# Kernel tuning notes

Measured on AMD Instinct MI355X. Metric: run time of the kernel, lower is better.

## Reference

```python
import jax, jax.numpy as jnp
import numpy as np

B, T, D, H = 2, 2048, 1024, 16
HD = D // H  # head dim = 64

def build_rope(t, half, base=10000.0):
    inv = 1.0 / (base ** (jnp.arange(0, half, dtype=jnp.float32) / half))
    ang = jnp.arange(t, dtype=jnp.float32)[:, None] * inv[None, :]  # (T, half)
    return jnp.stack([jnp.cos(ang), jnp.sin(ang)], axis=-1)  # (T, half, 2)

def setup_inputs() -> dict:
    key = jax.random.key(0)
    k1, k2, k3 = jax.random.split(key, 3)
    x = jax.random.normal(k1, (B, T, D), dtype=jnp.float32)
    W_attn = jax.random.normal(k2, (D, 3 * D), dtype=jnp.float32) * (1.0 / np.sqrt(D))
    W_proj = jax.random.normal(k3, (D, D), dtype=jnp.float32) * (1.0 / np.sqrt(D))
    rope = build_rope(T, HD // 2)
    mask = jnp.tril(jnp.ones((T, T), dtype=bool))[None, None]  # (1,1,T,T) causal
    return {"x": x, "rope": rope, "W_attn": W_attn, "W_proj": W_proj, "mask": mask}

def apply_rope(xq, rope):
    # xq: (B, T, H, HD); rope: (T, HD//2, 2)
    xs = xq.astype(jnp.float32).reshape(*xq.shape[:-1], -1, 2)        # (B,T,H,HD/2,2)
    rc = rope[:xq.shape[1]].reshape(1, xq.shape[1], 1, xs.shape[3], 2)  # (1,T,1,HD/2,2)
    out = jnp.stack([
        xs[..., 0] * rc[..., 0] - xs[..., 1] * rc[..., 1],
        xs[..., 1] * rc[..., 0] + xs[..., 0] * rc[..., 1],
    ], axis=-1)
    return out.reshape(xq.shape).astype(xq.dtype)

def reference(x, rope, W_attn, W_proj, mask):
    b, t, d = x.shape
    qkv = x @ W_attn                                   # (B,T,3D)
    q, k, v = jnp.split(qkv, 3, axis=2)
    q = apply_rope(q.reshape(b, t, H, HD), rope)
    k = apply_rope(k.reshape(b, t, H, HD), rope)
    v = v.reshape(b, t, H, HD)
    # (B,H,T,HD)
    q = q.transpose(0, 2, 1, 3)
    k = k.transpose(0, 2, 1, 3)
    v = v.transpose(0, 2, 1, 3)
    scale = 1.0 / np.sqrt(HD)
    scores = jnp.einsum('bhqd,bhkd->bhqk', q, k) * scale
    scores = jnp.where(mask, scores, jnp.finfo(scores.dtype).min)
    attn = jax.nn.softmax(scores, axis=-1)
    out = jnp.einsum('bhqk,bhkd->bhqd', attn, v)       # (B,H,T,HD)
    out = out.transpose(0, 2, 1, 3).reshape(b, t, d)
    return out @ W_proj
```

## Files before the change

kernel.cpp:

```cpp
#include <hip/hip_runtime.h>


typedef __bf16 bf16x8 __attribute__((ext_vector_type(8)));
typedef float f32x4 __attribute__((ext_vector_type(4)));

__device__ __forceinline__ float bf2f(unsigned short u) {
  unsigned int i = ((unsigned int)u) << 16;
  return __builtin_bit_cast(float, i);
}
__device__ __forceinline__ unsigned short f2bf(float f) {
  unsigned int i = __builtin_bit_cast(unsigned int, f);
  i += 0x7FFFu + ((i >> 16) & 1u);
  return (unsigned short)(i >> 16);
}
__device__ __forceinline__ unsigned int pack2(float a, float b) {
  return (unsigned int)f2bf(a) | ((unsigned int)f2bf(b) << 16);
}
__device__ __forceinline__ unsigned int cvtpk(float a, float b) {
  unsigned int r;
  asm("v_cvt_pk_bf16_f32 %0, %1, %2" : "=v"(r) : "v"(a), "v"(b));
  return r;
}

__device__ __forceinline__ void gload_lds16(const unsigned short* g, unsigned short* l) {
  __builtin_amdgcn_global_load_lds(
      (const __attribute__((address_space(1))) void*)g,
      (__attribute__((address_space(3))) void*)l, 16, 0, 0);
}

__global__ __launch_bounds__(256) void prep_kernel(
    const float* __restrict__ x, unsigned short* __restrict__ xb,
    const float* __restrict__ Wa, unsigned short* __restrict__ WaT,
    const float* __restrict__ Wp, unsigned short* __restrict__ WpT)
{
  __shared__ unsigned short tileT[64][72];
  const int bid = blockIdx.x, tid = threadIdx.x;

  if (bid < 2048) {
    int i = bid * 256 + tid;
    const float4 a0 = *reinterpret_cast<const float4*>(&x[(size_t)i * 8]);
    const float4 a1 = *reinterpret_cast<const float4*>(&x[(size_t)i * 8 + 4]);
    uint4 pk;
    pk.x = pack2(a0.x, a0.y);
    pk.y = pack2(a0.z, a0.w);
    pk.z = pack2(a1.x, a1.y);
    pk.w = pack2(a1.z, a1.w);
    *reinterpret_cast<uint4*>(&xb[(size_t)i * 8]) = pk;
    return;
  }
  const float* W;
  unsigned short* WT;
  int R, C, c0, r0;
  if (bid < 2816) {
    int tb = bid - 2048;
    W = Wa; WT = WaT; R = 1024; C = 3072;
    c0 = (tb % 48) * 64; r0 = (tb / 48) * 64;
  } else {
    int tb = bid - 2816;
    W = Wp; WT = WpT; R = 1024; C = 1024;
    c0 = (tb % 16) * 64; r0 = (tb / 16) * 64;
  }
  const int rr = tid >> 4, cc = (tid & 15) * 4;
#pragma unroll
  for (int it = 0; it < 4; ++it) {
    int gr = r0 + rr + it * 16;
    float4 v = *reinterpret_cast<const float4*>(&W[(size_t)gr * C + c0 + cc]);
    tileT[cc + 0][rr + it * 16] = f2bf(v.x);
    tileT[cc + 1][rr + it * 16] = f2bf(v.y);
    tileT[cc + 2][rr + it * 16] = f2bf(v.z);
    tileT[cc + 3][rr + it * 16] = f2bf(v.w);
  }
  __syncthreads();
  const int wc = tid >> 2, wk = (tid & 3) * 16;
  uint4 o0 = *reinterpret_cast<const uint4*>(&tileT[wc][wk]);
  uint4 o1 = *reinterpret_cast<const uint4*>(&tileT[wc][wk + 8]);
  unsigned short* dst = &WT[(size_t)(c0 + wc) * R + r0 + wk];
  *reinterpret_cast<uint4*>(dst) = o0;
  *reinterpret_cast<uint4*>(dst + 8) = o1;
}

__global__ __launch_bounds__(256) void gemm_qkv_kernel(
    const unsigned short* __restrict__ A, const unsigned short* __restrict__ BT,
    const float* __restrict__ rope,
    unsigned short* __restrict__ Qb, unsigned short* __restrict__ Kb,
    unsigned short* __restrict__ VT, int M, int N, int K)
{
  __shared__ alignas(16) unsigned short smem[16896];
  unsigned short* As = smem;
  unsigned short* Bs = smem + 4096;

  const int tid = threadIdx.x;
  const int nbx = gridDim.x;
  const int nwg = nbx * gridDim.y;
  const int orig = blockIdx.y * nbx + blockIdx.x;
  const int wg = (orig & 7) * (nwg >> 3) + (orig >> 3);
  const int m0 = (wg / nbx) * 128, n0 = (wg % nbx) * 128;

  const int w = tid >> 6, lane = tid & 63;
  const int wr = (w >> 1) * 64, wc = (w & 1) * 64;
  const int g = lane >> 4, r = lane & 15;

  f32x4 acc[4][4];
#pragma unroll
  for (int i = 0; i < 4; ++i)
#pragma unroll
    for (int j = 0; j < 4; ++j)
      acc[i][j] = f32x4{0.f, 0.f, 0.f, 0.f};

  const int srow = w * 32 + (lane >> 2);
  const int sk = (lane & 3) << 3;
  const size_t a_base = (size_t)(m0 + srow) * K + sk;
  const size_t b_base = (size_t)(n0 + srow) * K + sk;
  unsigned short* lA = &As[w * 1024 + lane * 8];
  unsigned short* lB = &Bs[w * 1024 + lane * 8];
  const size_t rstep = (size_t)16 * K;

  for (int k0 = 0; k0 < K; k0 += 32) {
    __syncthreads();
    gload_lds16(&A[a_base + k0], lA);
    gload_lds16(&A[a_base + k0 + rstep], lA + 512);
    gload_lds16(&BT[b_base + k0], lB);
    gload_lds16(&BT[b_base + k0 + rstep], lB + 512);
    __syncthreads();

    bf16x8 af[4], bff[4];
#pragma unroll
    for (int i = 0; i < 4; ++i)
      af[i] = __builtin_bit_cast(bf16x8,
          *reinterpret_cast<const uint4*>(&As[(wr + i * 16 + r) * 32 + g * 8]));
#pragma unroll
    for (int j = 0; j < 4; ++j)
      bff[j] = __builtin_bit_cast(bf16x8,
          *reinterpret_cast<const uint4*>(&Bs[(wc + j * 16 + r) * 32 + g * 8]));
#pragma unroll
    for (int i = 0; i < 4; ++i)
#pragma unroll
      for (int j = 0; j < 4; ++j)
        acc[i][j] = __builtin_amdgcn_mfma_f32_16x16x32_bf16(af[i], bff[j], acc[i][j], 0, 0, 0);
  }

  __syncthreads();
  unsigned short* ct = smem;
#pragma unroll
  for (int i = 0; i < 4; ++i)
#pragma unroll
    for (int j = 0; j < 4; ++j) {
      int row0 = wr + i * 16 + g * 4;
      int col  = wc + j * 16 + r;
      unsigned int w01 = cvtpk(acc[i][j][0], acc[i][j][1]);
      unsigned int w23 = cvtpk(acc[i][j][2], acc[i][j][3]);
      ct[(row0 + 0) * 132 + col] = (unsigned short)(w01 & 0xffffu);
      ct[(row0 + 1) * 132 + col] = (unsigned short)(w01 >> 16);
      ct[(row0 + 2) * 132 + col] = (unsigned short)(w23 & 0xffffu);
      ct[(row0 + 3) * 132 + col] = (unsigned short)(w23 >> 16);
    }
  __syncthreads();

  const int sec = n0 >> 10;
  if (sec < 2) {
    unsigned short* dstp = (sec == 0) ? Qb : Kb;
    const int prow = tid >> 4, pcol = (tid & 15) * 8;
    const int h = ((n0 & 1023) + pcol) >> 6;
    const int hd = pcol & 63;
#pragma unroll
    for (int p = 0; p < 8; ++p) {
      int row = p * 16 + prow;
      int rowM = m0 + row;
      int bb = rowM >> 11, tt = rowM & 2047;
      uint4 v = *reinterpret_cast<const uint4*>(&ct[row * 132 + pcol]);
      float x0 = bf2f((unsigned short)(v.x & 0xffffu)), x1 = bf2f((unsigned short)(v.x >> 16));
      float x2 = bf2f((unsigned short)(v.y & 0xffffu)), x3 = bf2f((unsigned short)(v.y >> 16));
      float x4 = bf2f((unsigned short)(v.z & 0xffffu)), x5 = bf2f((unsigned short)(v.z >> 16));
      float x6 = bf2f((unsigned short)(v.w & 0xffffu)), x7 = bf2f((unsigned short)(v.w >> 16));
      float4 rc0 = *reinterpret_cast<const float4*>(&rope[(size_t)tt * 64 + hd]);
      float4 rc1 = *reinterpret_cast<const float4*>(&rope[(size_t)tt * 64 + hd + 4]);
      float y0 = x0 * rc0.x - x1 * rc0.y, y1 = x1 * rc0.x + x0 * rc0.y;
      float y2 = x2 * rc0.z - x3 * rc0.w, y3 = x3 * rc0.z + x2 * rc0.w;
      float y4 = x4 * rc1.x - x5 * rc1.y, y5 = x5 * rc1.x + x4 * rc1.y;
      float y6 = x6 * rc1.z - x7 * rc1.w, y7 = x7 * rc1.z + x6 * rc1.w;
      uint4 o{cvtpk(y0, y1), cvtpk(y2, y3), cvtpk(y4, y5), cvtpk(y6, y7)};
      *reinterpret_cast<uint4*>(&dstp[((size_t)(bb * 16 + h) * 2048 + tt) * 64 + hd]) = o;
    }
  } else {
    const int col = tid >> 1, tch = (tid & 1) * 64;
    const int h = ((n0 - 2048) >> 6) + (col >> 6);
    const int hd = col & 63;
    const int bb = m0 >> 11, tt0 = m0 & 2047;
    unsigned short* vdst = &VT[((size_t)(bb * 16 + h) * 64 + hd) * 2048 + tt0 + tch];
#pragma unroll
    for (int j = 0; j < 8; ++j) {
      int t = tch + j * 8;
      unsigned int o0 = (unsigned int)ct[(t + 0) * 132 + col] | ((unsigned int)ct[(t + 1) * 132 + col] << 16);
      unsigned int o1 = (unsigned int)ct[(t + 2) * 132 + col] | ((unsigned int)ct[(t + 3) * 132 + col] << 16);
      unsigned int o2 = (unsigned int)ct[(t + 4) * 132 + col] | ((unsigned int)ct[(t + 5) * 132 + col] << 16);
      unsigned int o3 = (unsigned int)ct[(t + 6) * 132 + col] | ((unsigned int)ct[(t + 7) * 132 + col] << 16);
      *reinterpret_cast<uint4*>(&vdst[j * 8]) = uint4{o0, o1, o2, o3};
    }
  }
}

__global__ __launch_bounds__(256) void gemm_out_kernel(
    const unsigned short* __restrict__ A, const unsigned short* __restrict__ BT,
    float* __restrict__ Cp, int M, int N, int K)
{
  __shared__ alignas(16) unsigned short As[128 * 32];
  __shared__ alignas(16) unsigned short Bs[128 * 32];

  const int tid = threadIdx.x;
  const int nbx = gridDim.x;
  const int nwg = nbx * gridDim.y;
  const int orig = blockIdx.y * nbx + blockIdx.x;
  const int wg = (orig & 7) * (nwg >> 3) + (orig >> 3);
  const int m0 = (wg / nbx) * 128, n0 = (wg % nbx) * 128;

  const int w = tid >> 6, lane = tid & 63;
  const int wr = (w >> 1) * 64, wc = (w & 1) * 64;
  const int g = lane >> 4, r = lane & 15;

  f32x4 acc[4][4];
#pragma unroll
  for (int i = 0; i < 4; ++i)
#pragma unroll
    for (int j = 0; j < 4; ++j)
      acc[i][j] = f32x4{0.f, 0.f, 0.f, 0.f};

  const int srow = w * 32 + (lane >> 2);
  const int sk = (lane & 3) << 3;
  const size_t a_base = (size_t)(m0 + srow) * K + sk;
  const size_t b_base = (size_t)(n0 + srow) * K + sk;
  unsigned short* lA = &As[w * 1024 + lane * 8];
  unsigned short* lB = &Bs[w * 1024 + lane * 8];
  const size_t rstep = (size_t)16 * K;

  for (int k0 = 0; k0 < K; k0 += 32) {
    __syncthreads();
    gload_lds16(&A[a_base + k0], lA);
    gload_lds16(&A[a_base + k0 + rstep], lA + 512);
    gload_lds16(&BT[b_base + k0], lB);
    gload_lds16(&BT[b_base + k0 + rstep], lB + 512);
    __syncthreads();

    bf16x8 af[4], bff[4];
#pragma unroll
    for (int i = 0; i < 4; ++i)
      af[i] = __builtin_bit_cast(bf16x8,
          *reinterpret_cast<const uint4*>(&As[(wr + i * 16 + r) * 32 + g * 8]));
#pragma unroll
    for (int j = 0; j < 4; ++j)
      bff[j] = __builtin_bit_cast(bf16x8,
          *reinterpret_cast<const uint4*>(&Bs[(wc + j * 16 + r) * 32 + g * 8]));
#pragma unroll
    for (int i = 0; i < 4; ++i)
#pragma unroll
      for (int j = 0; j < 4; ++j)
        acc[i][j] = __builtin_amdgcn_mfma_f32_16x16x32_bf16(af[i], bff[j], acc[i][j], 0, 0, 0);
  }

#pragma unroll
  for (int i = 0; i < 4; ++i)
#pragma unroll
    for (int j = 0; j < 4; ++j)
#pragma unroll
      for (int reg = 0; reg < 4; ++reg) {
        int row = m0 + wr + i * 16 + g * 4 + reg;
        int col = n0 + wc + j * 16 + r;
        Cp[(size_t)row * N + col] = acc[i][j][reg];
      }
}

__global__ __launch_bounds__(512, 4) void attn_mfma_kernel(
    const unsigned short* __restrict__ Q, const unsigned short* __restrict__ K,
    const unsigned short* __restrict__ VT, unsigned short* __restrict__ O)
{
  __shared__ unsigned short Ks[2][64 * 64];
  __shared__ unsigned short Vs[2][64 * 64];

  const int bx = blockIdx.x;
  const int idx = bx & 255, hi = bx >> 8;
  const int bh = hi * 16 + (idx >> 4);
  const int tp = idx & 15;
  const int tile = hi ? tp : 15 - tp;
  const int b = bh >> 4, h = bh & 15;
  const size_t base = (size_t)bh * 2048 * 64;
  const unsigned short* VTb = VT + (size_t)bh * 64 * 2048;

  const int tid = threadIdx.x, w = tid >> 6, lane = tid & 63;
  const int g = lane >> 4, r = lane & 15;
  const int q0 = tile * 128;
  const int wrow0 = q0 + w * 16;

  bf16x8 qf[2];
#pragma unroll
  for (int kk = 0; kk < 2; ++kk)
    qf[kk] = __builtin_bit_cast(bf16x8, *reinterpret_cast<const uint4*>(
        &Q[base + (size_t)(wrow0 + r) * 64 + kk * 32 + g * 8]));

  float m = -1e30f, l = 0.f;
  f32x4 ov[4];
#pragma unroll
  for (int df = 0; df < 4; ++df) ov[df] = f32x4{0.f, 0.f, 0.f, 0.f};

  const int srow = tid >> 3, sc8 = (tid & 7) * 8;
  const unsigned short* Kg = &K[base + (size_t)srow * 64 + sc8];
  const unsigned short* Vg = &VTb[(size_t)srow * 2048 + sc8];
  const int sb = srow * 128 + ((sc8 * 2) ^ ((srow & 7) << 4));

  const float cs = 0.125f * 1.44269504f;
  const int nkt = (q0 >> 6) + 2;

  const int srcA = ((g & 1) << 5) | r;
  const int srcB = srcA | 16;
  const bool hsel = (g >> 1) != 0;

  uint4 kreg = *reinterpret_cast<const uint4*>(Kg);
  uint4 vreg = *reinterpret_cast<const uint4*>(Vg);
  *reinterpret_cast<uint4*>((char*)Ks[0] + sb) = kreg;
  *reinterpret_cast<uint4*>((char*)Vs[0] + sb) = vreg;
  __syncthreads();

  for (int c = 0; c < nkt; ++c) {
    const int kb = c * 64;
    const int cur = c & 1;
    const bool pfn = (c + 1 < nkt);
    if (pfn) {
      kreg = *reinterpret_cast<const uint4*>(Kg + (size_t)(kb + 64) * 64);
      vreg = *reinterpret_cast<const uint4*>(Vg + kb + 64);
    }

    if (kb <= wrow0 + 15) {
      f32x4 s[4];
#pragma unroll
      for (int cf = 0; cf < 4; ++cf) s[cf] = f32x4{0.f, 0.f, 0.f, 0.f};
      __builtin_amdgcn_s_setprio(1);
#pragma unroll
      for (int kk = 0; kk < 2; ++kk) {
#pragma unroll
        for (int cf = 0; cf < 4; ++cf) {
          int row = cf * 16 + r;
          const char* p = (const char*)Ks[cur] + row * 128 + ((kk * 64 + g * 16) ^ ((r & 7) << 4));
          bf16x8 kf = __builtin_bit_cast(bf16x8, *reinterpret_cast<const uint4*>(p));
          s[cf] = __builtin_amdgcn_mfma_f32_16x16x32_bf16(kf, qf[kk], s[cf], 0, 0, 0);
        }
      }
      __builtin_amdgcn_s_setprio(0);

      if (kb + 63 > wrow0) {
#pragma unroll
        for (int cf = 0; cf < 4; ++cf) {
          int keyb = kb + cf * 16 + g * 4;
#pragma unroll
          for (int reg = 0; reg < 4; ++reg)
            if (keyb + reg > wrow0 + r) s[cf][reg] = -1e30f;
        }
      }

      float vmx = s[0][0];
#pragma unroll
      for (int cf = 0; cf < 4; ++cf)
#pragma unroll
        for (int reg = 0; reg < 4; ++reg)
          vmx = fmaxf(vmx, s[cf][reg]);
      vmx = fmaxf(vmx, __shfl_xor(vmx, 16));
      vmx = fmaxf(vmx, __shfl_xor(vmx, 32));
      float mo = m;
      float mn, al;
      if (__all((vmx - mo) * cs <= 4.0f)) {
        mn = mo; al = 1.0f;
      } else {
        mn = fmaxf(mo, vmx);
        al = __builtin_amdgcn_exp2f((mo - mn) * cs);
        m = mn;
#pragma unroll
        for (int df = 0; df < 4; ++df) ov[df] *= al;
      }
      float ps = 0.f;
#pragma unroll
      for (int cf = 0; cf < 4; ++cf)
#pragma unroll
        for (int reg = 0; reg < 4; ++reg) {
          float p = __builtin_amdgcn_exp2f((s[cf][reg] - mn) * cs);
          s[cf][reg] = p;
          ps += p;
        }
      l = l * al + ps;

      unsigned int pk[4][2];
#pragma unroll
      for (int cf = 0; cf < 4; ++cf) {
        pk[cf][0] = cvtpk(s[cf][0], s[cf][1]);
        pk[cf][1] = cvtpk(s[cf][2], s[cf][3]);
      }

      __builtin_amdgcn_s_setprio(1);
#pragma unroll
      for (int kk = 0; kk < 2; ++kk) {
        unsigned int a0 = __shfl(pk[2 * kk][0], srcA), b0 = __shfl(pk[2 * kk + 1][0], srcA);
        unsigned int a1 = __shfl(pk[2 * kk][1], srcA), b1 = __shfl(pk[2 * kk + 1][1], srcA);
        unsigned int a2 = __shfl(pk[2 * kk][0], srcB), b2 = __shfl(pk[2 * kk + 1][0], srcB);
        unsigned int a3 = __shfl(pk[2 * kk][1], srcB), b3 = __shfl(pk[2 * kk + 1][1], srcB);
        uint4 pw{ hsel ? b0 : a0, hsel ? b1 : a1, hsel ? b2 : a2, hsel ? b3 : a3 };
        bf16x8 pf = __builtin_bit_cast(bf16x8, pw);
#pragma unroll
        for (int df = 0; df < 4; ++df) {
          int row = df * 16 + r;
          const char* p = (const char*)Vs[cur] + row * 128 + ((kk * 64 + g * 16) ^ ((r & 7) << 4));
          bf16x8 vf = __builtin_bit_cast(bf16x8, *reinterpret_cast<const uint4*>(p));
          ov[df] = __builtin_amdgcn_mfma_f32_16x16x32_bf16(vf, pf, ov[df], 0, 0, 0);
        }
      }
      __builtin_amdgcn_s_setprio(0);
    }

    if (pfn) {
      *reinterpret_cast<uint4*>((char*)Ks[cur ^ 1] + sb) = kreg;
      *reinterpret_cast<uint4*>((char*)Vs[cur ^ 1] + sb) = vreg;
    }
    __syncthreads();
  }

  float ls = l;
  ls += __shfl_xor(ls, 16);
  ls += __shfl_xor(ls, 32);
  float inv = 1.f / ls;
  size_t orow = (size_t)(b * 2048 + wrow0 + r) * 1024 + h * 64 + g * 4;
#pragma unroll
  for (int df = 0; df < 4; ++df) {
    uint2 o;
    o.x = cvtpk(ov[df][0] * inv, ov[df][1] * inv);
    o.y = cvtpk(ov[df][2] * inv, ov[df][3] * inv);
    *reinterpret_cast<uint2*>(&O[orow + df * 16]) = o;
  }
}

extern "C" void kernel_launch(void* const* d_in, const int* in_sizes, int n_in,
                              void* d_out, int out_size, void* d_ws, size_t ws_size,
                              hipStream_t stream)
{
  (void)in_sizes; (void)n_in; (void)out_size; (void)ws_size;
  const float* x    = (const float*)d_in[0];
  const float* rope = (const float*)d_in[1];
  const float* Wa   = (const float*)d_in[2];
  const float* Wp   = (const float*)d_in[3];

  unsigned short* ws  = (unsigned short*)d_ws;
  unsigned short* xb  = ws;
  unsigned short* WaT = xb  + (size_t)4096 * 1024;
  unsigned short* WpT = WaT + (size_t)1024 * 3072;
  unsigned short* Qb  = WpT + (size_t)1024 * 1024;
  unsigned short* Kb  = Qb  + (size_t)32 * 2048 * 64;
  unsigned short* VT  = Kb  + (size_t)32 * 2048 * 64;
  unsigned short* O   = VT  + (size_t)32 * 2048 * 64;
  float* out = (float*)d_out;

  prep_kernel<<<3072, 256, 0, stream>>>(x, xb, Wa, WaT, Wp, WpT);
  gemm_qkv_kernel<<<dim3(3072 / 128, 4096 / 128), 256, 0, stream>>>(
      xb, WaT, rope, Qb, Kb, VT, 4096, 3072, 1024);
  attn_mfma_kernel<<<512, 512, 0, stream>>>(Qb, Kb, VT, O);
  gemm_out_kernel<<<dim3(1024 / 128, 4096 / 128), 256, 0, stream>>>(
      O, WpT, out, 4096, 1024, 1024);
}
```

Before: 200.0 us.

## Widen attention key tiles to 128, reorder grid, stage output GEMM stores via LDS

The attention kernel now processes 128 keys per iteration instead of 64, doubling the K/V shared-memory tiles, the loads per stage and the score fragments per wave. This halves the barrier and loop count. The block index mapping changes to launch the heaviest causal tiles first across all heads. The output projection GEMM now writes its accumulators into padded LDS and stores them as coalesced float4 rows instead of scattered scalar stores. In exchange it uses more registers and LDS, which can lower occupancy, and the 67 KB static LDS buffer in the GEMM kernel may limit how many blocks fit per CU.

```diff
diff --git a/kernel.cpp b/kernel.cpp
--- a/kernel.cpp
+++ b/kernel.cpp
@@ -203,8 +203,9 @@
     const unsigned short* __restrict__ A, const unsigned short* __restrict__ BT,
     float* __restrict__ Cp, int M, int N, int K)
 {
-  __shared__ alignas(16) unsigned short As[128 * 32];
-  __shared__ alignas(16) unsigned short Bs[128 * 32];
+  __shared__ alignas(16) char smemc[67584];
+  unsigned short* As = (unsigned short*)smemc;
+  unsigned short* Bs = (unsigned short*)(smemc + 8192);
 
   const int tid = threadIdx.x;
   const int nbx = gridDim.x;
@@ -256,30 +257,35 @@
         acc[i][j] = __builtin_amdgcn_mfma_f32_16x16x32_bf16(af[i], bff[j], acc[i][j], 0, 0, 0);
   }
 
+  __syncthreads();
+  float* ct = (float*)smemc;
 #pragma unroll
   for (int i = 0; i < 4; ++i)
 #pragma unroll
     for (int j = 0; j < 4; ++j)
 #pragma unroll
-      for (int reg = 0; reg < 4; ++reg) {
-        int row = m0 + wr + i * 16 + g * 4 + reg;
-        int col = n0 + wc + j * 16 + r;
-        Cp[(size_t)row * N + col] = acc[i][j][reg];
-      }
+      for (int reg = 0; reg < 4; ++reg)
+        ct[(wr + i * 16 + g * 4 + reg) * 132 + wc + j * 16 + r] = acc[i][j][reg];
+  __syncthreads();
+  const int prow = tid >> 5, pcol = (tid & 31) * 4;
+#pragma unroll
+  for (int p = 0; p < 16; ++p) {
+    int row = p * 8 + prow;
+    float4 v = *reinterpret_cast<const float4*>(&ct[row * 132 + pcol]);
+    *reinterpret_cast<float4*>(&Cp[(size_t)(m0 + row) * N + n0 + pcol]) = v;
+  }
 }
 
 __global__ __launch_bounds__(512, 4) void attn_mfma_kernel(
     const unsigned short* __restrict__ Q, const unsigned short* __restrict__ K,
     const unsigned short* __restrict__ VT, unsigned short* __restrict__ O)
 {
-  __shared__ unsigned short Ks[2][64 * 64];
-  __shared__ unsigned short Vs[2][64 * 64];
+  __shared__ unsigned short Ks[2][128 * 64];
+  __shared__ unsigned short Vs[2][64 * 128];
 
   const int bx = blockIdx.x;
-  const int idx = bx & 255, hi = bx >> 8;
-  const int bh = hi * 16 + (idx >> 4);
-  const int tp = idx & 15;
-  const int tile = hi ? tp : 15 - tp;
+  const int tile = 15 - (bx >> 5);
+  const int bh = bx & 31;
   const int b = bh >> 4, h = bh & 15;
   const size_t base = (size_t)bh * 2048 * 64;
   const unsigned short* VTb = VT + (size_t)bh * 64 * 2048;
@@ -300,42 +306,50 @@
 #pragma unroll
   for (int df = 0; df < 4; ++df) ov[df] = f32x4{0.f, 0.f, 0.f, 0.f};
 
-  const int srow = tid >> 3, sc8 = (tid & 7) * 8;
-  const unsigned short* Kg = &K[base + (size_t)srow * 64 + sc8];
-  const unsigned short* Vg = &VTb[(size_t)srow * 2048 + sc8];
-  const int sb = srow * 128 + ((sc8 * 2) ^ ((srow & 7) << 4));
+  const int srowK = tid >> 3, sc8 = (tid & 7) * 8;
+  const unsigned short* Kg = &K[base + (size_t)srowK * 64 + sc8];
+  const int sbK = srowK * 128 + ((sc8 * 2) ^ ((srowK & 7) << 4));
+  const int d0 = tid >> 4, ck = (tid & 15) * 8;
+  const unsigned short* Vg = &VTb[(size_t)d0 * 2048 + ck];
+  const int sbV = d0 * 256 + ((ck * 2) ^ ((d0 & 7) << 4));
 
   const float cs = 0.125f * 1.44269504f;
-  const int nkt = (q0 >> 6) + 2;
+  const int nkt = tile + 1;
 
   const int srcA = ((g & 1) << 5) | r;
   const int srcB = srcA | 16;
-  const bool hsel = (g >> 1) != 0;
-
-  uint4 kreg = *reinterpret_cast<const uint4*>(Kg);
-  uint4 vreg = *reinterpret_cast<const uint4*>(Vg);
-  *reinterpret_cast<uint4*>((char*)Ks[0] + sb) = kreg;
-  *reinterpret_cast<uint4*>((char*)Vs[0] + sb) = vreg;
+  const int hsel = g >> 1;
+
+  uint4 k0r = *reinterpret_cast<const uint4*>(Kg);
+  uint4 k1r = *reinterpret_cast<const uint4*>(Kg + (size_t)64 * 64);
+  uint4 v0r = *reinterpret_cast<const uint4*>(Vg);
+  uint4 v1r = *reinterpret_cast<const uint4*>(Vg + (size_t)32 * 2048);
+  *reinterpret_cast<uint4*>((char*)Ks[0] + sbK) = k0r;
+  *reinterpret_cast<uint4*>((char*)Ks[0] + sbK + 8192) = k1r;
+  *reinterpret_cast<uint4*>((char*)Vs[0] + sbV) = v0r;
+  *reinterpret_cast<uint4*>((char*)Vs[0] + sbV + 8192) = v1r;
   __syncthreads();
 
   for (int c = 0; c < nkt; ++c) {
-    const int kb = c * 64;
+    const int kb = c * 128;
     const int cur = c & 1;
     const bool pfn = (c + 1 < nkt);
     if (pfn) {
-      kreg = *reinterpret_cast<const uint4*>(Kg + (size_t)(kb + 64) * 64);
-      vreg = *reinterpret_cast<const uint4*>(Vg + kb + 64);
+      k0r = *reinterpret_cast<const uint4*>(Kg + (size_t)(kb + 128) * 64);
+      k1r = *reinterpret_cast<const uint4*>(Kg + (size_t)(kb + 192) * 64);
+      v0r = *reinterpret_cast<const uint4*>(Vg + kb + 128);
+      v1r = *reinterpret_cast<const uint4*>(Vg + (size_t)32 * 2048 + kb + 128);
     }
 
     if (kb <= wrow0 + 15) {
-      f32x4 s[4];
-#pragma unroll
-      for (int cf = 0; cf < 4; ++cf) s[cf] = f32x4{0.f, 0.f, 0.f, 0.f};
+      f32x4 s[8];
+#pragma unroll
+      for (int cf = 0; cf < 8; ++cf) s[cf] = f32x4{0.f, 0.f, 0.f, 0.f};
       __builtin_amdgcn_s_setprio(1);
 #pragma unroll
       for (int kk = 0; kk < 2; ++kk) {
 #pragma unroll
-        for (int cf = 0; cf < 4; ++cf) {
+        for (int cf = 0; cf < 8; ++cf) {
           int row = cf * 16 + r;
           const char* p = (const char*)Ks[cur] + row * 128 + ((kk * 64 + g * 16) ^ ((r & 7) << 4));
           bf16x8 kf = __builtin_bit_cast(bf16x8, *reinterpret_cast<const uint4*>(p));
@@ -344,9 +358,9 @@
       }
       __builtin_amdgcn_s_setprio(0);
 
-      if (kb + 63 > wrow0) {
-#pragma unroll
-        for (int cf = 0; cf < 4; ++cf) {
+      if (kb + 127 > wrow0) {
+#pragma unroll
+        for (int cf = 0; cf < 8; ++cf) {
           int keyb = kb + cf * 16 + g * 4;
 #pragma unroll
           for (int reg = 0; reg < 4; ++reg)
@@ -356,7 +370,7 @@
 
       float vmx = s[0][0];
 #pragma unroll
-      for (int cf = 0; cf < 4; ++cf)
+      for (int cf = 0; cf < 8; ++cf)
 #pragma unroll
         for (int reg = 0; reg < 4; ++reg)
           vmx = fmaxf(vmx, s[cf][reg]);
@@ -375,7 +389,7 @@
       }
       float ps = 0.f;
 #pragma unroll
-      for (int cf = 0; cf < 4; ++cf)
+      for (int cf = 0; cf < 8; ++cf)
 #pragma unroll
         for (int reg = 0; reg < 4; ++reg) {
           float p = __builtin_amdgcn_exp2f((s[cf][reg] - mn) * cs);
@@ -384,16 +398,16 @@
         }
       l = l * al + ps;
 
-      unsigned int pk[4][2];
-#pragma unroll
-      for (int cf = 0; cf < 4; ++cf) {
+      unsigned int pk[8][2];
+#pragma unroll
+      for (int cf = 0; cf < 8; ++cf) {
         pk[cf][0] = cvtpk(s[cf][0], s[cf][1]);
         pk[cf][1] = cvtpk(s[cf][2], s[cf][3]);
       }
 
       __builtin_amdgcn_s_setprio(1);
 #pragma unroll
-      for (int kk = 0; kk < 2; ++kk) {
+      for (int kk = 0; kk < 4; ++kk) {
         unsigned int a0 = __shfl(pk[2 * kk][0], srcA), b0 = __shfl(pk[2 * kk + 1][0], srcA);
         unsigned int a1 = __shfl(pk[2 * kk][1], srcA), b1 = __shfl(pk[2 * kk + 1][1], srcA);
         unsigned int a2 = __shfl(pk[2 * kk][0], srcB), b2 = __shfl(pk[2 * kk + 1][0], srcB);
@@ -403,7 +417,7 @@
 #pragma unroll
         for (int df = 0; df < 4; ++df) {
           int row = df * 16 + r;
-          const char* p = (const char*)Vs[cur] + row * 128 + ((kk * 64 + g * 16) ^ ((r & 7) << 4));
+          const char* p = (const char*)Vs[cur] + row * 256 + ((kk * 64 + g * 16) ^ ((r & 7) << 4));
           bf16x8 vf = __builtin_bit_cast(bf16x8, *reinterpret_cast<const uint4*>(p));
           ov[df] = __builtin_amdgcn_mfma_f32_16x16x32_bf16(vf, pf, ov[df], 0, 0, 0);
         }
@@ -412,8 +426,10 @@
     }
 
     if (pfn) {
-      *reinterpret_cast<uint4*>((char*)Ks[cur ^ 1] + sb) = kreg;
-      *reinterpret_cast<uint4*>((char*)Vs[cur ^ 1] + sb) = vreg;
+      *reinterpret_cast<uint4*>((char*)Ks[cur ^ 1] + sbK) = k0r;
+      *reinterpret_cast<uint4*>((char*)Ks[cur ^ 1] + sbK + 8192) = k1r;
+      *reinterpret_cast<uint4*>((char*)Vs[cur ^ 1] + sbV) = v0r;
+      *reinterpret_cast<uint4*>((char*)Vs[cur ^ 1] + sbV + 8192) = v1r;
     }
     __syncthreads();
   }
```

New measurement: 209.4 us. 4.7% more time.
